# Kernel optimization log

Hardware: AMD Instinct MI355X
Metric: run time of the kernel (lower is better)

## Reference

```python
import jax, jax.numpy as jnp
import numpy as np
from jax import lax

N, LOOKBACK, FEAT, HID, HORIZON = 8000, 12, 64, 128, 4
DENSITY = 0.002  # ~16 avg in-degree


def setup_inputs() -> dict:
    key = jax.random.key(0)
    ks = jax.random.split(key, 20)
    tspan = jnp.arange(HORIZON, dtype=jnp.float32)
    x = jax.random.normal(ks[0], (LOOKBACK, N, FEAT), dtype=jnp.float32)
    # sparse weighted adjacency: nonzero pattern with ~DENSITY fill
    mask = (jax.random.uniform(ks[1], (N, N)) < DENSITY).astype(jnp.float32)
    adj_w = mask * jax.random.uniform(ks[2], (N, N), dtype=jnp.float32)

    def lin(k, fi, fo):
        s = 1.0 / np.sqrt(fi)
        return jax.random.uniform(k, (fi, fo), minval=-s, maxval=s, dtype=jnp.float32)

    return {
        "tspan": tspan, "x": x, "adj_w": adj_w,
        # init_enc: Linear(lookback->hid), ReLU, Linear(hid->1)
        "We1": lin(ks[3], LOOKBACK, HID), "be1": jnp.zeros((HID,), jnp.float32),
        "We2": lin(ks[4], HID, 1), "be2": jnp.zeros((1,), jnp.float32),
        # f: Linear(feat->hid), ReLU, Linear(hid->feat)
        "Wf1": lin(ks[5], FEAT, HID), "bf1": jnp.zeros((HID,), jnp.float32),
        "Wf2": lin(ks[6], HID, FEAT), "bf2": jnp.zeros((FEAT,), jnp.float32),
        # SAGEConv1 (feat->hid): lin_l (aggr, with bias), lin_r (root, no bias)
        "Wl1": lin(ks[7], FEAT, HID), "bl1": jnp.zeros((HID,), jnp.float32),
        "Wr1": lin(ks[8], FEAT, HID),
        # SAGEConv2 (hid->feat)
        "Wl2": lin(ks[9], HID, FEAT), "bl2": jnp.zeros((FEAT,), jnp.float32),
        "Wr2": lin(ks[10], HID, FEAT),
    }


def reference(tspan, x, adj_w, We1, be1, We2, be2, Wf1, bf1, Wf2, bf2,
              Wl1, bl1, Wr1, Wl2, bl2, Wr2):
    # binarized adjacency from nonzero pattern (adj.nonzero() in torch)
    A = (adj_w != 0).astype(x.dtype)                      # [N, N], edge (i,j) => msg x[i] -> node j
    deg = jnp.maximum(A.sum(axis=0), 1.0)                 # in-degree per target [N]

    def sage(h, Wl, bl, Wr):
        aggr = (A.T @ h) / deg[:, None]                   # mean over in-neighbors
        return aggr @ Wl + bl + h @ Wr

    def dxdt(h):
        x_self = jax.nn.relu(h @ Wf1 + bf1) @ Wf2 + bf2
        x_neigh = sage(jax.nn.relu(sage(h, Wl1, bl1, Wr1)), Wl2, bl2, Wr2)
        return jnp.clip(x_self + x_neigh, -1000.0, 1000.0)

    # init_enc: [L,N,F] -> permute [N,F,L] -> MLP over lookback -> [N,F]
    xe = jnp.transpose(x, (1, 2, 0))                      # [N, F, L]
    x0 = (jax.nn.relu(xe @ We1 + be1) @ We2 + be2)[..., 0]  # [N, F]

    # fixed-step Euler at tspan points (torchdiffeq method='euler')
    dts = tspan[1:] - tspan[:-1]

    def step(h, dt):
        hn = h + dt * dxdt(h)
        return hn, hn

    _, xs = lax.scan(step, x0, dts)
    return jnp.concatenate([x0[None], xs], axis=0)        # [horizon, N, F]
```

## Files before the change

### kernel.cpp

```cpp
#include <hip/hip_runtime.h>

#define N_NODES 8000
#define FEAT 64
#define HID 128
#define LOOKBACK 12
#define CAP 64

__global__ __launch_bounds__(256)
void front_kernel(int* __restrict__ cnt,
                  const float* __restrict__ x,
                  const float* __restrict__ We1, const float* __restrict__ be1,
                  const float* __restrict__ We2, const float* __restrict__ be2,
                  float* __restrict__ out0,
                  const float* __restrict__ Wl1, const float* __restrict__ Wr1,
                  const float* __restrict__ Wl2, const float* __restrict__ Wr2,
                  float* __restrict__ Ws1, float* __restrict__ Wc2) {
    __shared__ float sW1T[HID * LOOKBACK];
    __shared__ float sB1[HID];
    __shared__ float sW2[HID];
    const int tid = threadIdx.x;
    if (tid < 16) cnt[blockIdx.x * 16 + tid] = 0;
    {
        const int gid = blockIdx.x * 256 + tid;
        if (gid < 128 * 128) {
            int k = gid >> 7, j = gid & 127;
            Ws1[gid] = (k < 64) ? Wl1[k * 128 + j] : Wr1[(k - 64) * 128 + j];
        } else if (gid < 2 * 128 * 128) {
            int w = gid - 128 * 128;
            int k = w >> 7, j = w & 127;
            Wc2[w] = (j < 64) ? Wl2[k * 64 + j] : Wr2[k * 64 + (j - 64)];
        }
    }
    for (int e = tid; e < HID * LOOKBACK; e += 256) {
        int l = e / HID, h = e % HID;
        sW1T[h * LOOKBACK + l] = We1[e];
    }
    for (int e = tid; e < HID; e += 256) { sB1[e] = be1[e]; sW2[e] = We2[e]; }
    __syncthreads();
    int g = (blockIdx.x * 256 + tid) * 4;
    float xv[4][LOOKBACK];
    #pragma unroll
    for (int l = 0; l < LOOKBACK; ++l) {
        float4 v = *reinterpret_cast<const float4*>(x + (long)l * N_NODES * FEAT + g);
        xv[0][l] = v.x; xv[1][l] = v.y; xv[2][l] = v.z; xv[3][l] = v.w;
    }
    float b2 = be2[0];
    float acc[4] = {b2, b2, b2, b2};
    for (int h = 0; h < HID; ++h) {
        float s0 = sB1[h], s1 = s0, s2 = s0, s3 = s0;
        #pragma unroll
        for (int l = 0; l < LOOKBACK; ++l) {
            float w = sW1T[h * LOOKBACK + l];
            s0 += xv[0][l] * w; s1 += xv[1][l] * w;
            s2 += xv[2][l] * w; s3 += xv[3][l] * w;
        }
        float w2 = sW2[h];
        acc[0] += fmaxf(s0, 0.0f) * w2; acc[1] += fmaxf(s1, 0.0f) * w2;
        acc[2] += fmaxf(s2, 0.0f) * w2; acc[3] += fmaxf(s3, 0.0f) * w2;
    }
    float4 o = {acc[0], acc[1], acc[2], acc[3]};
    *reinterpret_cast<float4*>(out0 + g) = o;
}

__global__ __launch_bounds__(256)
void build_adj_kernel(const float* __restrict__ adj, int* __restrict__ cnt,
                      int* __restrict__ lists) {
    const long NQ = (long)N_NODES * N_NODES / 4;
    const long STRIDE = 2048L * 256;
    const long t = (long)blockIdx.x * 256 + threadIdx.x;

    int lc = 0;
    int e0 = 0, e1 = 0, e2 = 0, e3 = 0, e4 = 0;
    int e5 = 0, e6 = 0, e7 = 0, e8 = 0, e9 = 0;

    #pragma unroll 1
    for (long q = t; q < NQ; q += STRIDE) {
        float4 w = *reinterpret_cast<const float4*>(adj + 4 * q);
        if (w.x != 0.0f || w.y != 0.0f || w.z != 0.0f || w.w != 0.0f) {
            float wv[4] = {w.x, w.y, w.z, w.w};
            #pragma unroll
            for (int c = 0; c < 4; ++c) {
                if (wv[c] != 0.0f) {
                    int e = (int)(q * 4 + c);
                    if      (lc == 0) e0 = e;
                    else if (lc == 1) e1 = e;
                    else if (lc == 2) e2 = e;
                    else if (lc == 3) e3 = e;
                    else if (lc == 4) e4 = e;
                    else if (lc == 5) e5 = e;
                    else if (lc == 6) e6 = e;
                    else if (lc == 7) e7 = e;
                    else if (lc == 8) e8 = e;
                    else if (lc == 9) e9 = e;
                    ++lc;
                }
            }
        }
    }
    #define DRAIN(K, EK)                                                     \
        if (lc > K) {                                                        \
            int ii = (EK) / N_NODES;                                         \
            int jj = (EK) % N_NODES;                                         \
            int p = atomicAdd(&cnt[jj], 1);                                  \
            if (p < CAP) lists[(long)jj * CAP + p] = ii;                     \
        }
    DRAIN(0, e0) DRAIN(1, e1) DRAIN(2, e2) DRAIN(3, e3) DRAIN(4, e4)
    DRAIN(5, e5) DRAIN(6, e6) DRAIN(7, e7) DRAIN(8, e8) DRAIN(9, e9)
    #undef DRAIN
}

__global__ __launch_bounds__(256)
void sageproj_kernel(const float* __restrict__ h,
                     int* __restrict__ lists, int* __restrict__ cnt,
                     float* __restrict__ degf, int do_sort,
                     const float* __restrict__ Ws1, const float* __restrict__ bl1,
                     const float* __restrict__ Wc2, const float* __restrict__ bl2,
                     const float* __restrict__ Wf1, const float* __restrict__ bf1,
                     const float* __restrict__ Wf2, const float* __restrict__ bf2,
                     float* __restrict__ pl, float* __restrict__ q) {
    __shared__ float v[16][132];
    __shared__ float rr[16][132];
    __shared__ float tt[16][132];
    __shared__ float xsl[16][68];
    __shared__ float wbuf[64 * 128];
    const int tid = threadIdx.x;
    const int nb = blockIdx.x * 16;
    if (do_sort) {
        const int wv = tid >> 6, lane = tid & 63;
        #pragma unroll 1
        for (int r = 0; r < 4; ++r) {
            const int n = nb + wv * 4 + r;
            int m = cnt[n]; if (m > CAP) m = CAP;
            int val = (lane < m) ? lists[(long)n * CAP + lane] : 0x7FFFFFFF;
            #pragma unroll
            for (int k = 2; k <= 64; k <<= 1) {
                #pragma unroll
                for (int j = k >> 1; j > 0; j >>= 1) {
                    int other = __shfl_xor(val, j);
                    bool keepMin = (((lane & j) == 0) == ((lane & k) == 0));
                    int mn = val < other ? val : other;
                    int mx = val < other ? other : val;
                    val = keepMin ? mn : mx;
                }
            }
            lists[(long)n * CAP + lane] = val;
            if (lane == 0) { cnt[n] = m; degf[n] = (float)(m > 0 ? m : 1); }
        }
        __syncthreads();
    }
    const int ln = tid >> 4, jg = tid & 15;
    const int n = nb + ln;
    const int c0 = jg * 4;
    {
        const int m = cnt[n];
        const int* l = lists + (long)n * CAP;
        const float inv = 1.0f / degf[n];
        float4 a = {0, 0, 0, 0};
        for (int e = 0; e < m; ++e) {
            float4 b = *reinterpret_cast<const float4*>(h + (long)l[e] * FEAT + c0);
            a.x += b.x; a.y += b.y; a.z += b.z; a.w += b.w;
        }
        float4 av = {a.x * inv, a.y * inv, a.z * inv, a.w * inv};
        *reinterpret_cast<float4*>(&v[ln][c0]) = av;
        *reinterpret_cast<float4*>(&v[ln][64 + c0]) =
            *reinterpret_cast<const float4*>(h + (long)n * FEAT + c0);
    }
    {
        float4 b0 = *reinterpret_cast<const float4*>(bl1 + c0);
        float4 b1 = *reinterpret_cast<const float4*>(bl1 + 64 + c0);
        float A0[4] = {b0.x, b0.y, b0.z, b0.w};
        float A1[4] = {b1.x, b1.y, b1.z, b1.w};
        for (int kc = 0; kc < 2; ++kc) {
            __syncthreads();
            for (int e = tid; e < 2048; e += 256)
                *(reinterpret_cast<float4*>(wbuf) + e) =
                    *(reinterpret_cast<const float4*>(Ws1 + kc * 8192) + e);
            __syncthreads();
            #pragma unroll 4
            for (int k = 0; k < 64; ++k) {
                float a = v[ln][kc * 64 + k];
                float4 w0 = *reinterpret_cast<const float4*>(&wbuf[k * 128 + c0]);
                float4 w1 = *reinterpret_cast<const float4*>(&wbuf[k * 128 + 64 + c0]);
                A0[0] += a * w0.x; A0[1] += a * w0.y; A0[2] += a * w0.z; A0[3] += a * w0.w;
                A1[0] += a * w1.x; A1[1] += a * w1.y; A1[2] += a * w1.z; A1[3] += a * w1.w;
            }
        }
        float4 o0 = {fmaxf(A0[0],0.f), fmaxf(A0[1],0.f), fmaxf(A0[2],0.f), fmaxf(A0[3],0.f)};
        float4 o1 = {fmaxf(A1[0],0.f), fmaxf(A1[1],0.f), fmaxf(A1[2],0.f), fmaxf(A1[3],0.f)};
        *reinterpret_cast<float4*>(&rr[ln][c0]) = o0;
        *reinterpret_cast<float4*>(&rr[ln][64 + c0]) = o1;
    }
    {
        float4 b0 = *reinterpret_cast<const float4*>(bf1 + c0);
        float4 b1 = *reinterpret_cast<const float4*>(bf1 + 64 + c0);
        float A0[4] = {b0.x, b0.y, b0.z, b0.w};
        float A1[4] = {b1.x, b1.y, b1.z, b1.w};
        __syncthreads();
        for (int e = tid; e < 2048; e += 256)
            *(reinterpret_cast<float4*>(wbuf) + e) =
                *(reinterpret_cast<const float4*>(Wf1) + e);
        __syncthreads();
        #pragma unroll 4
        for (int k = 0; k < 64; ++k) {
            float a = v[ln][64 + k];
            float4 w0 = *reinterpret_cast<const float4*>(&wbuf[k * 128 + c0]);
            float4 w1 = *reinterpret_cast<const float4*>(&wbuf[k * 128 + 64 + c0]);
            A0[0] += a * w0.x; A0[1] += a * w0.y; A0[2] += a * w0.z; A0[3] += a * w0.w;
            A1[0] += a * w1.x; A1[1] += a * w1.y; A1[2] += a * w1.z; A1[3] += a * w1.w;
        }
        float4 o0 = {fmaxf(A0[0],0.f), fmaxf(A0[1],0.f), fmaxf(A0[2],0.f), fmaxf(A0[3],0.f)};
        float4 o1 = {fmaxf(A1[0],0.f), fmaxf(A1[1],0.f), fmaxf(A1[2],0.f), fmaxf(A1[3],0.f)};
        *reinterpret_cast<float4*>(&tt[ln][c0]) = o0;
        *reinterpret_cast<float4*>(&tt[ln][64 + c0]) = o1;
    }
    {
        float4 b0 = *reinterpret_cast<const float4*>(bf2 + c0);
        float X[4] = {b0.x, b0.y, b0.z, b0.w};
        __syncthreads();
        for (int e = tid; e < 2048; e += 256)
            *(reinterpret_cast<float4*>(wbuf) + e) =
                *(reinterpret_cast<const float4*>(Wf2) + e);
        __syncthreads();
        #pragma unroll 4
        for (int k = 0; k < 128; ++k) {
            float a = tt[ln][k];
            float4 w = *reinterpret_cast<const float4*>(&wbuf[k * 64 + c0]);
            X[0] += a * w.x; X[1] += a * w.y; X[2] += a * w.z; X[3] += a * w.w;
        }
        float4 o = {X[0], X[1], X[2], X[3]};
        *reinterpret_cast<float4*>(&xsl[ln][c0]) = o;
    }
    {
        float P0[4] = {0, 0, 0, 0};
        float P1[4] = {0, 0, 0, 0};
        for (int kc = 0; kc < 2; ++kc) {
            __syncthreads();
            for (int e = tid; e < 2048; e += 256)
                *(reinterpret_cast<float4*>(wbuf) + e) =
                    *(reinterpret_cast<const float4*>(Wc2 + kc * 8192) + e);
            __syncthreads();
            #pragma unroll 4
            for (int k = 0; k < 64; ++k) {
                float a = rr[ln][kc * 64 + k];
                float4 w0 = *reinterpret_cast<const float4*>(&wbuf[k * 128 + c0]);
                float4 w1 = *reinterpret_cast<const float4*>(&wbuf[k * 128 + 64 + c0]);
                P0[0] += a * w0.x; P0[1] += a * w0.y; P0[2] += a * w0.z; P0[3] += a * w0.w;
                P1[0] += a * w1.x; P1[1] += a * w1.y; P1[2] += a * w1.z; P1[3] += a * w1.w;
            }
        }
        float4 op = {P0[0], P0[1], P0[2], P0[3]};
        *reinterpret_cast<float4*>(pl + (long)n * FEAT + c0) = op;
        float4 bv = *reinterpret_cast<const float4*>(bl2 + c0);
        float4 oq = {P1[0] + bv.x + xsl[ln][c0 + 0],
                     P1[1] + bv.y + xsl[ln][c0 + 1],
                     P1[2] + bv.z + xsl[ln][c0 + 2],
                     P1[3] + bv.w + xsl[ln][c0 + 3]};
        *reinterpret_cast<float4*>(q + (long)n * FEAT + c0) = oq;
    }
}

__global__ __launch_bounds__(256)
void epi_kernel(const float* __restrict__ pl, const float* __restrict__ q,
                const int* __restrict__ lists, const int* __restrict__ cnt,
                const float* __restrict__ degf, const float* __restrict__ hcur,
                const float* __restrict__ tspan, int step,
                float* __restrict__ hnext) {
    const int tid = threadIdx.x;
    const int ln = tid >> 4, sub = tid & 15;
    const int n = blockIdx.x * 16 + ln;
    const int f0 = sub * 4;
    const int m = cnt[n];
    const int* l = lists + (long)n * CAP;
    const float inv = 1.0f / degf[n];
    float4 a = {0, 0, 0, 0};
    for (int e = 0; e < m; ++e) {
        float4 b = *reinterpret_cast<const float4*>(pl + (long)l[e] * FEAT + f0);
        a.x += b.x; a.y += b.y; a.z += b.z; a.w += b.w;
    }
    const float dt = tspan[step + 1] - tspan[step];
    float4 qv = *reinterpret_cast<const float4*>(q + (long)n * FEAT + f0);
    float4 hv = *reinterpret_cast<const float4*>(hcur + (long)n * FEAT + f0);
    float s0 = qv.x + a.x * inv, s1 = qv.y + a.y * inv;
    float s2 = qv.z + a.z * inv, s3 = qv.w + a.w * inv;
    s0 = fminf(fmaxf(s0, -1000.f), 1000.f); s1 = fminf(fmaxf(s1, -1000.f), 1000.f);
    s2 = fminf(fmaxf(s2, -1000.f), 1000.f); s3 = fminf(fmaxf(s3, -1000.f), 1000.f);
    float4 o = {hv.x + dt * s0, hv.y + dt * s1, hv.z + dt * s2, hv.w + dt * s3};
    *reinterpret_cast<float4*>(hnext + (long)n * FEAT + f0) = o;
}

extern "C" void kernel_launch(void* const* d_in, const int* in_sizes, int n_in,
                              void* d_out, int out_size, void* d_ws, size_t ws_size,
                              hipStream_t stream) {
    const float* tspan = (const float*)d_in[0];
    const float* x     = (const float*)d_in[1];
    const float* adj   = (const float*)d_in[2];
    const float* We1   = (const float*)d_in[3];
    const float* be1   = (const float*)d_in[4];
    const float* We2   = (const float*)d_in[5];
    const float* be2   = (const float*)d_in[6];
    const float* Wf1   = (const float*)d_in[7];
    const float* bf1   = (const float*)d_in[8];
    const float* Wf2   = (const float*)d_in[9];
    const float* bf2   = (const float*)d_in[10];
    const float* Wl1   = (const float*)d_in[11];
    const float* bl1   = (const float*)d_in[12];
    const float* Wr1   = (const float*)d_in[13];
    const float* Wl2   = (const float*)d_in[14];
    const float* bl2   = (const float*)d_in[15];
    const float* Wr2   = (const float*)d_in[16];
    float* out = (float*)d_out;

    char* ws = (char*)d_ws;
    int*   lists = (int*)  (ws + 0);
    int*   cnt   = (int*)  (ws + 2048000);
    float* degf  = (float*)(ws + 2080000);
    float* Ws1   = (float*)(ws + 2112000);
    float* Wc2   = (float*)(ws + 2177536);
    float* pl    = (float*)(ws + 2243072);
    float* q     = (float*)(ws + 4291072);

    front_kernel<<<500, 256, 0, stream>>>(cnt, x, We1, be1, We2, be2, out,
                                          Wl1, Wr1, Wl2, Wr2, Ws1, Wc2);
    build_adj_kernel<<<2048, 256, 0, stream>>>(adj, cnt, lists);

    for (int s = 0; s < 3; ++s) {
        const float* hcur  = out + (long)s       * N_NODES * FEAT;
        float*       hnext = out + (long)(s + 1) * N_NODES * FEAT;
        sageproj_kernel<<<500, 256, 0, stream>>>(hcur, lists, cnt, degf, (s == 0) ? 1 : 0,
                                                 Ws1, bl1, Wc2, bl2,
                                                 Wf1, bf1, Wf2, bf2, pl, q);
        epi_kernel<<<500, 256, 0, stream>>>(pl, q, lists, cnt, degf, hcur, tspan, s, hnext);
    }
}
```

Baseline: 242.1 us.

## Halve nodes per block in sageproj and remap threads for more parallelism

The fused SAGE/MLP projection kernel now handles 8 nodes per block instead of 16 and launches 1000 blocks instead of 500. Weight staging is split into 16KB chunks, so shared memory per block drops and more blocks can be resident per CU. Each thread now computes 4 outputs instead of 8, and activations are read as float4. The aggregation and Wf2 stages use only half the threads. The trade-off is twice as much total weight staging into LDS across the grid, plus more barriers per block.

```diff
diff --git a/kernel.cpp b/kernel.cpp
--- a/kernel.cpp
+++ b/kernel.cpp
@@ -118,18 +118,18 @@
                      const float* __restrict__ Wf1, const float* __restrict__ bf1,
                      const float* __restrict__ Wf2, const float* __restrict__ bf2,
                      float* __restrict__ pl, float* __restrict__ q) {
-    __shared__ float v[16][132];
-    __shared__ float rr[16][132];
-    __shared__ float tt[16][132];
-    __shared__ float xsl[16][68];
-    __shared__ float wbuf[64 * 128];
+    __shared__ float v[8][132];
+    __shared__ float rr[8][132];
+    __shared__ float tt[8][132];
+    __shared__ float xsl[8][68];
+    __shared__ float wbuf[32 * 128];
     const int tid = threadIdx.x;
-    const int nb = blockIdx.x * 16;
+    const int nb = blockIdx.x * 8;
     if (do_sort) {
         const int wv = tid >> 6, lane = tid & 63;
         #pragma unroll 1
-        for (int r = 0; r < 4; ++r) {
-            const int n = nb + wv * 4 + r;
+        for (int r = 0; r < 2; ++r) {
+            const int n = nb + wv * 2 + r;
             int m = cnt[n]; if (m > CAP) m = CAP;
             int val = (lane < m) ? lists[(long)n * CAP + lane] : 0x7FFFFFFF;
             #pragma unroll
@@ -148,115 +148,132 @@
         }
         __syncthreads();
     }
-    const int ln = tid >> 4, jg = tid & 15;
-    const int n = nb + ln;
-    const int c0 = jg * 4;
-    {
+    if (tid < 128) {
+        const int ln = tid >> 4, sub = tid & 15;
+        const int n = nb + ln;
+        const int f0 = sub * 4;
         const int m = cnt[n];
         const int* l = lists + (long)n * CAP;
         const float inv = 1.0f / degf[n];
         float4 a = {0, 0, 0, 0};
         for (int e = 0; e < m; ++e) {
-            float4 b = *reinterpret_cast<const float4*>(h + (long)l[e] * FEAT + c0);
+            float4 b = *reinterpret_cast<const float4*>(h + (long)l[e] * FEAT + f0);
             a.x += b.x; a.y += b.y; a.z += b.z; a.w += b.w;
         }
         float4 av = {a.x * inv, a.y * inv, a.z * inv, a.w * inv};
-        *reinterpret_cast<float4*>(&v[ln][c0]) = av;
-        *reinterpret_cast<float4*>(&v[ln][64 + c0]) =
-            *reinterpret_cast<const float4*>(h + (long)n * FEAT + c0);
-    }
+        *reinterpret_cast<float4*>(&v[ln][f0]) = av;
+        *reinterpret_cast<float4*>(&v[ln][64 + f0]) =
+            *reinterpret_cast<const float4*>(h + (long)n * FEAT + f0);
+    }
+    const int jg = tid & 31, ln = tid >> 5;
+    const int c0 = jg * 4;
+    #define STAGE(SRCPTR, OFF4)                                              \
+        do {                                                                 \
+            __syncthreads();                                                 \
+            for (int e = tid; e < 1024; e += 256)                            \
+                *(reinterpret_cast<float4*>(wbuf) + e) =                     \
+                    *(reinterpret_cast<const float4*>(SRCPTR) + (OFF4) + e); \
+            __syncthreads();                                                 \
+        } while (0)
     {
         float4 b0 = *reinterpret_cast<const float4*>(bl1 + c0);
-        float4 b1 = *reinterpret_cast<const float4*>(bl1 + 64 + c0);
-        float A0[4] = {b0.x, b0.y, b0.z, b0.w};
-        float A1[4] = {b1.x, b1.y, b1.z, b1.w};
+        float A[4] = {b0.x, b0.y, b0.z, b0.w};
+        for (int kc = 0; kc < 4; ++kc) {
+            STAGE(Ws1, kc * 1024);
+            #pragma unroll 4
+            for (int k4 = 0; k4 < 8; ++k4) {
+                float4 av = *reinterpret_cast<const float4*>(&v[ln][kc * 32 + k4 * 4]);
+                const float aa[4] = {av.x, av.y, av.z, av.w};
+                #pragma unroll
+                for (int kk = 0; kk < 4; ++kk) {
+                    float4 w = *reinterpret_cast<const float4*>(&wbuf[(k4 * 4 + kk) * 128 + c0]);
+                    float a = aa[kk];
+                    A[0] += a * w.x; A[1] += a * w.y; A[2] += a * w.z; A[3] += a * w.w;
+                }
+            }
+        }
+        float4 o = {fmaxf(A[0],0.f), fmaxf(A[1],0.f), fmaxf(A[2],0.f), fmaxf(A[3],0.f)};
+        *reinterpret_cast<float4*>(&rr[ln][c0]) = o;
+    }
+    {
+        float4 b0 = *reinterpret_cast<const float4*>(bf1 + c0);
+        float A[4] = {b0.x, b0.y, b0.z, b0.w};
         for (int kc = 0; kc < 2; ++kc) {
-            __syncthreads();
-            for (int e = tid; e < 2048; e += 256)
-                *(reinterpret_cast<float4*>(wbuf) + e) =
-                    *(reinterpret_cast<const float4*>(Ws1 + kc * 8192) + e);
-            __syncthreads();
+            STAGE(Wf1, kc * 1024);
             #pragma unroll 4
-            for (int k = 0; k < 64; ++k) {
-                float a = v[ln][kc * 64 + k];
-                float4 w0 = *reinterpret_cast<const float4*>(&wbuf[k * 128 + c0]);
-                float4 w1 = *reinterpret_cast<const float4*>(&wbuf[k * 128 + 64 + c0]);
-                A0[0] += a * w0.x; A0[1] += a * w0.y; A0[2] += a * w0.z; A0[3] += a * w0.w;
-                A1[0] += a * w1.x; A1[1] += a * w1.y; A1[2] += a * w1.z; A1[3] += a * w1.w;
-            }
-        }
-        float4 o0 = {fmaxf(A0[0],0.f), fmaxf(A0[1],0.f), fmaxf(A0[2],0.f), fmaxf(A0[3],0.f)};
-        float4 o1 = {fmaxf(A1[0],0.f), fmaxf(A1[1],0.f), fmaxf(A1[2],0.f), fmaxf(A1[3],0.f)};
-        *reinterpret_cast<float4*>(&rr[ln][c0]) = o0;
-        *reinterpret_cast<float4*>(&rr[ln][64 + c0]) = o1;
-    }
-    {
-        float4 b0 = *reinterpret_cast<const float4*>(bf1 + c0);
-        float4 b1 = *reinterpret_cast<const float4*>(bf1 + 64 + c0);
-        float A0[4] = {b0.x, b0.y, b0.z, b0.w};
-        float A1[4] = {b1.x, b1.y, b1.z, b1.w};
-        __syncthreads();
-        for (int e = tid; e < 2048; e += 256)
-            *(reinterpret_cast<float4*>(wbuf) + e) =
-                *(reinterpret_cast<const float4*>(Wf1) + e);
-        __syncthreads();
-        #pragma unroll 4
-        for (int k = 0; k < 64; ++k) {
-            float a = v[ln][64 + k];
-            float4 w0 = *reinterpret_cast<const float4*>(&wbuf[k * 128 + c0]);
-            float4 w1 = *reinterpret_cast<const float4*>(&wbuf[k * 128 + 64 + c0]);
-            A0[0] += a * w0.x; A0[1] += a * w0.y; A0[2] += a * w0.z; A0[3] += a * w0.w;
-            A1[0] += a * w1.x; A1[1] += a * w1.y; A1[2] += a * w1.z; A1[3] += a * w1.w;
-        }
-        float4 o0 = {fmaxf(A0[0],0.f), fmaxf(A0[1],0.f), fmaxf(A0[2],0.f), fmaxf(A0[3],0.f)};
-        float4 o1 = {fmaxf(A1[0],0.f), fmaxf(A1[1],0.f), fmaxf(A1[2],0.f), fmaxf(A1[3],0.f)};
-        *reinterpret_cast<float4*>(&tt[ln][c0]) = o0;
-        *reinterpret_cast<float4*>(&tt[ln][64 + c0]) = o1;
-    }
-    {
-        float4 b0 = *reinterpret_cast<const float4*>(bf2 + c0);
-        float X[4] = {b0.x, b0.y, b0.z, b0.w};
-        __syncthreads();
-        for (int e = tid; e < 2048; e += 256)
-            *(reinterpret_cast<float4*>(wbuf) + e) =
-                *(reinterpret_cast<const float4*>(Wf2) + e);
-        __syncthreads();
-        #pragma unroll 4
-        for (int k = 0; k < 128; ++k) {
-            float a = tt[ln][k];
-            float4 w = *reinterpret_cast<const float4*>(&wbuf[k * 64 + c0]);
-            X[0] += a * w.x; X[1] += a * w.y; X[2] += a * w.z; X[3] += a * w.w;
-        }
-        float4 o = {X[0], X[1], X[2], X[3]};
-        *reinterpret_cast<float4*>(&xsl[ln][c0]) = o;
-    }
-    {
-        float P0[4] = {0, 0, 0, 0};
-        float P1[4] = {0, 0, 0, 0};
+            for (int k4 = 0; k4 < 8; ++k4) {
+                float4 av = *reinterpret_cast<const float4*>(&v[ln][64 + kc * 32 + k4 * 4]);
+                const float aa[4] = {av.x, av.y, av.z, av.w};
+                #pragma unroll
+                for (int kk = 0; kk < 4; ++kk) {
+                    float4 w = *reinterpret_cast<const float4*>(&wbuf[(k4 * 4 + kk) * 128 + c0]);
+                    float a = aa[kk];
+                    A[0] += a * w.x; A[1] += a * w.y; A[2] += a * w.z; A[3] += a * w.w;
+                }
+            }
+        }
+        float4 o = {fmaxf(A[0],0.f), fmaxf(A[1],0.f), fmaxf(A[2],0.f), fmaxf(A[3],0.f)};
+        *reinterpret_cast<float4*>(&tt[ln][c0]) = o;
+    }
+    {
+        const int ln3 = tid >> 4, c3 = (tid & 15) * 4;
+        const bool act3 = tid < 128;
+        float A[4];
+        if (act3) {
+            float4 b0 = *reinterpret_cast<const float4*>(bf2 + c3);
+            A[0] = b0.x; A[1] = b0.y; A[2] = b0.z; A[3] = b0.w;
+        }
         for (int kc = 0; kc < 2; ++kc) {
-            __syncthreads();
-            for (int e = tid; e < 2048; e += 256)
-                *(reinterpret_cast<float4*>(wbuf) + e) =
-                    *(reinterpret_cast<const float4*>(Wc2 + kc * 8192) + e);
-            __syncthreads();
+            STAGE(Wf2, kc * 1024);
+            if (act3) {
+                #pragma unroll 4
+                for (int k4 = 0; k4 < 16; ++k4) {
+                    float4 av = *reinterpret_cast<const float4*>(&tt[ln3][kc * 64 + k4 * 4]);
+                    const float aa[4] = {av.x, av.y, av.z, av.w};
+                    #pragma unroll
+                    for (int kk = 0; kk < 4; ++kk) {
+                        float4 w = *reinterpret_cast<const float4*>(&wbuf[(k4 * 4 + kk) * 64 + c3]);
+                        float a = aa[kk];
+                        A[0] += a * w.x; A[1] += a * w.y; A[2] += a * w.z; A[3] += a * w.w;
+                    }
+                }
+            }
+        }
+        if (act3) {
+            float4 o = {A[0], A[1], A[2], A[3]};
+            *reinterpret_cast<float4*>(&xsl[ln3][c3]) = o;
+        }
+    }
+    {
+        float A[4] = {0, 0, 0, 0};
+        for (int kc = 0; kc < 4; ++kc) {
+            STAGE(Wc2, kc * 1024);
             #pragma unroll 4
-            for (int k = 0; k < 64; ++k) {
-                float a = rr[ln][kc * 64 + k];
-                float4 w0 = *reinterpret_cast<const float4*>(&wbuf[k * 128 + c0]);
-                float4 w1 = *reinterpret_cast<const float4*>(&wbuf[k * 128 + 64 + c0]);
-                P0[0] += a * w0.x; P0[1] += a * w0.y; P0[2] += a * w0.z; P0[3] += a * w0.w;
-                P1[0] += a * w1.x; P1[1] += a * w1.y; P1[2] += a * w1.z; P1[3] += a * w1.w;
-            }
-        }
-        float4 op = {P0[0], P0[1], P0[2], P0[3]};
-        *reinterpret_cast<float4*>(pl + (long)n * FEAT + c0) = op;
-        float4 bv = *reinterpret_cast<const float4*>(bl2 + c0);
-        float4 oq = {P1[0] + bv.x + xsl[ln][c0 + 0],
-                     P1[1] + bv.y + xsl[ln][c0 + 1],
-                     P1[2] + bv.z + xsl[ln][c0 + 2],
-                     P1[3] + bv.w + xsl[ln][c0 + 3]};
-        *reinterpret_cast<float4*>(q + (long)n * FEAT + c0) = oq;
-    }
+            for (int k4 = 0; k4 < 8; ++k4) {
+                float4 av = *reinterpret_cast<const float4*>(&rr[ln][kc * 32 + k4 * 4]);
+                const float aa[4] = {av.x, av.y, av.z, av.w};
+                #pragma unroll
+                for (int kk = 0; kk < 4; ++kk) {
+                    float4 w = *reinterpret_cast<const float4*>(&wbuf[(k4 * 4 + kk) * 128 + c0]);
+                    float a = aa[kk];
+                    A[0] += a * w.x; A[1] += a * w.y; A[2] += a * w.z; A[3] += a * w.w;
+                }
+            }
+        }
+        if (jg < 16) {
+            float4 o = {A[0], A[1], A[2], A[3]};
+            *reinterpret_cast<float4*>(pl + (long)(nb + ln) * FEAT + c0) = o;
+        } else {
+            const int cq = c0 - 64;
+            float4 bv = *reinterpret_cast<const float4*>(bl2 + cq);
+            float4 o = {A[0] + bv.x + xsl[ln][cq + 0],
+                        A[1] + bv.y + xsl[ln][cq + 1],
+                        A[2] + bv.z + xsl[ln][cq + 2],
+                        A[3] + bv.w + xsl[ln][cq + 3]};
+            *reinterpret_cast<float4*>(q + (long)(nb + ln) * FEAT + cq) = o;
+        }
+    }
+    #undef STAGE
 }
 
 __global__ __launch_bounds__(256)
@@ -326,9 +343,9 @@
     for (int s = 0; s < 3; ++s) {
         const float* hcur  = out + (long)s       * N_NODES * FEAT;
         float*       hnext = out + (long)(s + 1) * N_NODES * FEAT;
-        sageproj_kernel<<<500, 256, 0, stream>>>(hcur, lists, cnt, degf, (s == 0) ? 1 : 0,
-                                                 Ws1, bl1, Wc2, bl2,
-                                                 Wf1, bf1, Wf2, bf2, pl, q);
+        sageproj_kernel<<<1000, 256, 0, stream>>>(hcur, lists, cnt, degf, (s == 0) ? 1 : 0,
+                                                  Ws1, bl1, Wc2, bl2,
+                                                  Wf1, bf1, Wf2, bf2, pl, q);
         epi_kernel<<<500, 256, 0, stream>>>(pl, q, lists, cnt, degf, hcur, tspan, s, hnext);
     }
 }
```

Result: slower. 253.7 us (+4.8%).
